# Performance work log

Hardware: AMD Instinct MI355X
Metric: run time of the kernel (lower is better)

Reference implementation:

```python
import jax, jax.numpy as jnp
import numpy as np

H = 1024        # hidden_units
NH = 16         # num_heads
HD = H // NH    # head_dim = 64
B = 32
S = 500
MAX_SEQ = 500
ROPE_BASE = 10000.0


def setup_inputs() -> dict:
    key = jax.random.key(0)
    ks = jax.random.split(key, 16)
    s = 1.0 / np.sqrt(H)
    inp = {
        "query": jax.random.normal(ks[0], (B, S, H), jnp.float32),
        "key":   jax.random.normal(ks[1], (B, S, H), jnp.float32),
        "value": jax.random.normal(ks[2], (B, S, H), jnp.float32),
        "attn_mask": jax.random.randint(ks[3], (B, S), 0, 2).astype(bool),
        "Wq": jax.random.uniform(ks[4], (H, H), jnp.float32, -s, s),
        "bq": jax.random.uniform(ks[5], (H,), jnp.float32, -s, s),
        "Wk": jax.random.uniform(ks[6], (H, H), jnp.float32, -s, s),
        "bk": jax.random.uniform(ks[7], (H,), jnp.float32, -s, s),
        "Wv": jax.random.uniform(ks[8], (H, H), jnp.float32, -s, s),
        "bv": jax.random.uniform(ks[9], (H,), jnp.float32, -s, s),
        "Wo": jax.random.uniform(ks[10], (H, H), jnp.float32, -s, s),
        "bo": jax.random.uniform(ks[11], (H,), jnp.float32, -s, s),
        # rel_pos_bias embedding table: [2*max_seq_len-1, num_heads]
        "rel_emb": jax.random.normal(ks[12], (2 * MAX_SEQ - 1, NH), jnp.float32),
    }
    return inp


def _rope_tables(seq_len, head_dim, dtype):
    inv_freq = 1.0 / (ROPE_BASE ** (jnp.arange(0, head_dim, 2, dtype=jnp.float32) / head_dim))
    t = jnp.arange(seq_len, dtype=jnp.float32)
    freqs = t[:, None] * inv_freq[None, :]           # [S, HD/2]
    emb = jnp.concatenate([freqs, freqs], axis=-1)   # [S, HD]
    return jnp.cos(emb).astype(dtype), jnp.sin(emb).astype(dtype)


def _apply_rope(x, cos, sin):
    # x: [B, NH, S, HD]; even/odd slicing variant from source
    x_rot = jnp.concatenate([-x[..., 1::2], x[..., 0::2]], axis=-1)
    return x * cos + x_rot * sin


def reference(query, key, value, attn_mask, Wq, bq, Wk, bk, Wv, bv, Wo, bo, rel_emb):
    b, s, _ = query.shape
    Q = (query @ Wq.T + bq).reshape(b, s, NH, HD).transpose(0, 2, 1, 3)  # [B,NH,S,HD]
    K = (key   @ Wk.T + bk).reshape(b, s, NH, HD).transpose(0, 2, 1, 3)
    V = (value @ Wv.T + bv).reshape(b, s, NH, HD).transpose(0, 2, 1, 3)

    cos, sin = _rope_tables(s, HD, Q.dtype)  # [S,HD]
    Q = _apply_rope(Q, cos, sin)
    K = _apply_rope(K, cos, sin)

    # relative-position bias: [1, NH, S, S]
    pos = jnp.arange(s)[:, None] - jnp.arange(s)[None, :]
    rel_idx = jnp.clip(pos + MAX_SEQ - 1, 0, 2 * MAX_SEQ - 2)
    rel_bias = rel_emb[rel_idx].transpose(2, 0, 1)[None]  # [1,NH,S,S]

    # key-padding mask -> additive float mask [B,1,1,S]
    mask_bias = jnp.where(attn_mask[:, None, None, :], 0.0, -jnp.inf).astype(Q.dtype)

    scale = 1.0 / np.sqrt(HD)
    scores = jnp.einsum('bhqd,bhkd->bhqk', Q, K) * scale + mask_bias + rel_bias
    attn = jax.nn.softmax(scores, axis=-1)
    out = jnp.einsum('bhqk,bhkd->bhqd', attn, V)
    out = out.transpose(0, 2, 1, 3).reshape(b, s, H)
    out = jnp.clip(out, -30.0, 30.0)
    return out @ Wo.T + bo
```

## Files before the change

### kernel.cpp

```cpp
#include <hip/hip_runtime.h>
#include <math.h>


typedef unsigned short u16;
typedef unsigned int   u32;
typedef unsigned char  u8;
using bf16x8 = __attribute__((ext_vector_type(8))) short;
using f32x4  = __attribute__((ext_vector_type(4))) float;
using f32x2  = __attribute__((ext_vector_type(2))) float;
using u16x4  = __attribute__((ext_vector_type(4))) unsigned short;

#define DEV __device__ __forceinline__

#if __has_builtin(__builtin_amdgcn_exp2f)
#define EXP2(x) __builtin_amdgcn_exp2f(x)
#else
#define EXP2(x) exp2f(x)
#endif

DEV u16 f2bf(float f) {
  union { float f; u32 u; } c; c.f = f;
  u32 u = c.u;
  return (u16)((u + 0x7FFFu + ((u >> 16) & 1u)) >> 16);
}
DEV float bf2f(u16 h) {
  union { u32 u; float f; } c; c.u = ((u32)h) << 16;
  return c.f;
}
DEV u32 cvtpk(float a, float b) {
  u32 r;
  asm("v_cvt_pk_bf16_f32 %0, %1, %2" : "=v"(r) : "v"(a), "v"(b));
  return r;
}

DEV void async16(void* l, const void* g) {
  __builtin_amdgcn_global_load_lds(
      (__attribute__((address_space(1))) unsigned int*)g,
      (__attribute__((address_space(3))) unsigned int*)l, 16, 0, 0);
}

__global__ __launch_bounds__(512) void build_gather(const void* __restrict__ mraw,
                                                    u16* __restrict__ karr,
                                                    int* __restrict__ kept) {
  const int b = blockIdx.x;
  const int t = threadIdx.x;
  const int lane = t & 63, wave = t >> 6;
  __shared__ int s_li, s_lf;
  __shared__ int wbase[8];
  __shared__ int wpop[8];
  if (t == 0) { s_li = 0; s_lf = 0; }
  __syncthreads();
  const u32* w = (const u32*)mraw;
  int li = 0, lf = 0;
  for (int g = t; g < 4000; g += 512) {
    u32 v = w[g];
    li |= !(v == 0u || v == 1u);
    lf |= !(v == 0u || v == 0x3F800000u);
  }
  if (li) atomicOr(&s_li, 1);
  if (lf) atomicOr(&s_lf, 1);
  __syncthreads();
  const int mode = (!s_li) ? 0 : ((!s_lf) ? 1 : 2);
  int v = 0;
  if (t < 500) {
    if (mode == 0)      v = ((const int*)mraw)[b * 500 + t] != 0;
    else if (mode == 1) v = (((const float*)mraw)[b * 500 + t] != 0.0f);
    else                v = ((const u8*)mraw)[b * 500 + t] != 0;
  }
  unsigned long long bal = __ballot(v != 0);
  karr[b * 512 + t] = 0xFFFF;
  if (lane == 0) wpop[wave] = __popcll(bal);
  __syncthreads();
  if (t == 0) {
    int s = 0;
    for (int ww = 0; ww < 8; ++ww) { wbase[ww] = s; s += wpop[ww]; }
    kept[b] = s;
  }
  __syncthreads();
  if (v) {
    int rank = wbase[wave] + __popcll(bal & ((1ull << lane) - 1ull));
    karr[b * 512 + rank] = (u16)t;
  }
}

__global__ __launch_bounds__(256) void rope_table(float* __restrict__ tab) {
  int idx = blockIdx.x * 256 + threadIdx.x;
  if (idx >= 16000) return;
  int s = idx >> 5, j = idx & 31;
  float ang = (float)s * exp2f(-(float)j * 0.41524100f);
  float sn, cs;
  sincosf(ang, &sn, &cs);
  tab[idx * 2] = cs;
  tab[idx * 2 + 1] = sn;
}

__global__ __launch_bounds__(256) void cvt_w4(const float* __restrict__ w0,
                                              const float* __restrict__ w1,
                                              const float* __restrict__ w2,
                                              const float* __restrict__ w3,
                                              u16* __restrict__ dst) {
  const float* src = (blockIdx.y == 0) ? w0 : (blockIdx.y == 1) ? w1
                    : (blockIdx.y == 2) ? w2 : w3;
  int i = blockIdx.x * 256 + threadIdx.x;
  f32x4 f = *(const f32x4*)(src + (size_t)i * 4);
  u16x4 o;
  o[0] = f2bf(f[0]); o[1] = f2bf(f[1]); o[2] = f2bf(f[2]); o[3] = f2bf(f[3]);
  *(u16x4*)(dst + (size_t)blockIdx.y * 1048576 + (size_t)i * 4) = o;
}

__global__ __launch_bounds__(256) void cvt_f32_bf16(const float* __restrict__ src,
                                                    u16* __restrict__ dst, int n4) {
  int i = blockIdx.x * 256 + threadIdx.x;
  int stride = gridDim.x * 256;
  for (; i < n4; i += stride) {
    f32x4 f = *(const f32x4*)(src + (size_t)i * 4);
    u16x4 o;
    o[0] = f2bf(f[0]); o[1] = f2bf(f[1]); o[2] = f2bf(f[2]); o[3] = f2bf(f[3]);
    *(u16x4*)(dst + (size_t)i * 4) = o;
  }
}

__global__ __launch_bounds__(256) void gathercvt2(const float* __restrict__ srcK,
                                                  const float* __restrict__ srcV,
                                                  const u16* __restrict__ karr,
                                                  const int* __restrict__ kept,
                                                  u16* __restrict__ dstK,
                                                  u16* __restrict__ dstV) {
  const int b = blockIdx.y;
  const int r = blockIdx.x * 2 + (threadIdx.x >> 7);
  if (r >= kept[b]) return;
  const float* src = blockIdx.z ? srcV : srcK;
  u16* dst = blockIdx.z ? dstV : dstK;
  const int c = (threadIdx.x & 127) * 8;
  const int tok = karr[b * 512 + r];
  const float* s = src + ((size_t)b * 500 + tok) * 1024 + c;
  f32x4 f0 = *(const f32x4*)s;
  f32x4 f1 = *(const f32x4*)(s + 4);
  u16 o[8];
  o[0] = f2bf(f0[0]); o[1] = f2bf(f0[1]); o[2] = f2bf(f0[2]); o[3] = f2bf(f0[3]);
  o[4] = f2bf(f1[0]); o[5] = f2bf(f1[1]); o[6] = f2bf(f1[2]); o[7] = f2bf(f1[3]);
  *(bf16x8*)(dst + ((size_t)b * 512 + r) * 1024 + c) = *(bf16x8*)o;
}

template <int MODE>
__global__ __launch_bounds__(512, 2) void gemm_bt(const u16* __restrict__ A,
                                                  const u16* __restrict__ Bw,
                                                  const float* __restrict__ bias,
                                                  void* __restrict__ Cout, int M,
                                                  const float* __restrict__ tabg,
                                                  const int* __restrict__ keptp) {
  const int bid = blockIdx.x;
  int m0, n0, Mloc;
  size_t abase, crowbase;
  if (MODE == 3) {
    const int swz = (bid & 7) * 32 + (bid >> 3);
    const int mb = swz >> 2;
    n0 = (swz & 3) * 256;
    const int b = mb >> 1, rb = mb & 1;
    const int kb = keptp[b];
    if (rb * 256 >= kb) return;
    m0 = rb * 256;
    Mloc = kb;
    abase = (size_t)b * 512 * 1024;
    crowbase = (size_t)b * 512;
  } else {
    const int xcd = bid & 7, idx = bid >> 3;
    const int swz = (xcd < 4 ? xcd * 32 : 128 + (xcd - 4) * 31) + idx;
    m0 = (swz >> 2) * 256;
    n0 = (swz & 3) * 256;
    Mloc = M;
    abase = 0;
    crowbase = 0;
  }
  const int tid = threadIdx.x;
  const int wave = tid >> 6;
  const int wr = wave >> 2, wc = wave & 3;
  const int fr = tid & 15, fo = (tid >> 4) & 3;
  const int sl0 = (fo ^ (fr & 7)) * 8;
  const int sl1 = ((4 + fo) ^ (fr & 7)) * 8;

  __shared__ __attribute__((aligned(16))) u16 AS[2 * 16384];
  __shared__ __attribute__((aligned(16))) u16 BS[2 * 16384];

  f32x4 acc[8][4];
#pragma unroll
  for (int mi = 0; mi < 8; ++mi)
#pragma unroll
    for (int ni = 0; ni < 4; ++ni)
#pragma unroll
      for (int j = 0; j < 4; ++j) acc[mi][ni][j] = 0.f;

  auto STG = [&](int t, int buf) {
    u16* sA = &AS[buf * 16384];
    u16* sB = &BS[buf * 16384];
#pragma unroll
    for (int i = 0; i < 4; ++i) {
      int c = i * 512 + tid;
      int r = c >> 3, v = (c & 7) ^ (r & 7);
      int ar = min(m0 + r, Mloc - 1);
      async16(&sA[c * 8], A + abase + (size_t)ar * 1024 + t * 64 + v * 8);
    }
#pragma unroll
    for (int i = 0; i < 4; ++i) {
      int c = i * 512 + tid;
      int r = c >> 3, v = (c & 7) ^ (r & 7);
      async16(&sB[c * 8], Bw + (size_t)(n0 + r) * 1024 + t * 64 + v * 8);
    }
  };

  STG(0, 0);
  asm volatile("s_waitcnt vmcnt(0)" ::: "memory");
  __builtin_amdgcn_sched_barrier(0);
  __builtin_amdgcn_s_barrier();

  int cur = 0;
  for (int t = 0; t < 16; ++t) {
    if (t + 1 < 16) STG(t + 1, cur ^ 1);
    const u16* a0 = &AS[cur * 16384];
    const u16* b0 = &BS[cur * 16384];
    bf16x8 a[8], b[4];
#pragma unroll
    for (int mi = 0; mi < 8; ++mi)
      a[mi] = *(const bf16x8*)&a0[(wr * 128 + mi * 16 + fr) * 64 + sl0];
#pragma unroll
    for (int ni = 0; ni < 4; ++ni)
      b[ni] = *(const bf16x8*)&b0[(wc * 64 + ni * 16 + fr) * 64 + sl0];
    asm volatile("s_waitcnt lgkmcnt(0)" ::: "memory");
    __builtin_amdgcn_sched_barrier(0);
    __builtin_amdgcn_s_setprio(1);
#pragma unroll
    for (int mi = 0; mi < 8; ++mi)
#pragma unroll
      for (int ni = 0; ni < 4; ++ni)
        acc[mi][ni] = __builtin_amdgcn_mfma_f32_16x16x32_bf16(a[mi], b[ni], acc[mi][ni], 0, 0, 0);
    __builtin_amdgcn_s_setprio(0);
#pragma unroll
    for (int mi = 0; mi < 8; ++mi)
      a[mi] = *(const bf16x8*)&a0[(wr * 128 + mi * 16 + fr) * 64 + sl1];
#pragma unroll
    for (int ni = 0; ni < 4; ++ni)
      b[ni] = *(const bf16x8*)&b0[(wc * 64 + ni * 16 + fr) * 64 + sl1];
    asm volatile("s_waitcnt lgkmcnt(0)" ::: "memory");
    __builtin_amdgcn_sched_barrier(0);
    __builtin_amdgcn_s_setprio(1);
#pragma unroll
    for (int mi = 0; mi < 8; ++mi)
#pragma unroll
      for (int ni = 0; ni < 4; ++ni)
        acc[mi][ni] = __builtin_amdgcn_mfma_f32_16x16x32_bf16(a[mi], b[ni], acc[mi][ni], 0, 0, 0);
    __builtin_amdgcn_s_setprio(0);
    asm volatile("s_waitcnt vmcnt(0)" ::: "memory");
    __builtin_amdgcn_sched_barrier(0);
    __builtin_amdgcn_s_barrier();
    cur ^= 1;
  }

  __syncthreads();
  if (MODE == 2) {
    float* fw = (float*)&AS[0] + wave * 1024;
    const int hh = (n0 >> 6) + wc;
    const int lane = tid & 63;
    const int row = lane >> 2;
    const int jb = (lane & 3) * 8;
    float bvv[4];
#pragma unroll
    for (int ni = 0; ni < 4; ++ni) bvv[ni] = bias[n0 + wc * 64 + ni * 16 + fr];
#pragma unroll
    for (int mi = 0; mi < 8; ++mi) {
#pragma unroll
      for (int ni = 0; ni < 4; ++ni)
#pragma unroll
        for (int r = 0; r < 4; ++r)
          fw[(fo * 4 + r) * 64 + ni * 16 + fr] = acc[mi][ni][r] + bvv[ni];
      int m = m0 + wr * 128 + mi * 16 + row;
      if (m < Mloc) {
        int bb = (u32)m / 500u;
        int ss = m - bb * 500;
        u16* dst = (u16*)Cout + (((size_t)(bb * 16 + hh)) * 500 + ss) * 64;
        bf16x8 va, vb;
#pragma unroll
        for (int p = 0; p < 8; ++p) {
          int j = jb + p;
          float x0 = fw[row * 64 + j];
          float x1 = fw[row * 64 + 32 + j];
          float xe = fw[row * 64 + 2 * j];
          float xo = fw[row * 64 + 2 * j + 1];
          f32x2 cn = *(const f32x2*)(tabg + (ss * 32 + j) * 2);
          va[p] = (short)f2bf(x0 * cn[0] - xo * cn[1]);
          vb[p] = (short)f2bf(x1 * cn[0] + xe * cn[1]);
        }
        *(bf16x8*)(dst + jb) = va;
        *(bf16x8*)(dst + 32 + jb) = vb;
      }
      __builtin_amdgcn_s_barrier();
    }
  } else if (MODE == 1 || MODE == 3) {
    u16* bw = (u16*)&AS[0] + wave * 2048;
#pragma unroll
    for (int mi = 0; mi < 8; ++mi) {
#pragma unroll
      for (int ni = 0; ni < 4; ++ni) {
        float bv = bias[n0 + wc * 64 + ni * 16 + fr];
#pragma unroll
        for (int r = 0; r < 4; ++r)
          bw[(fo * 4 + r) * 64 + ni * 16 + fr] = f2bf(acc[mi][ni][r] + bv);
      }
      int lane = tid & 63;
      int ro = lane >> 2, ch = lane & 3;
      int m = m0 + wr * 128 + mi * 16 + ro;
      bf16x8 v0 = *(const bf16x8*)&bw[ro * 64 + ch * 16];
      bf16x8 v1 = *(const bf16x8*)&bw[ro * 64 + ch * 16 + 8];
      if (m < Mloc) {
        u16* dst = (u16*)Cout + (crowbase + m) * 1024 + n0 + wc * 64 + ch * 16;
        *(bf16x8*)dst = v0;
        *(bf16x8*)(dst + 8) = v1;
      }
    }
  } else {
    float* fw = (float*)&AS[0] + wave * 1024;
#pragma unroll
    for (int mi = 0; mi < 8; ++mi) {
#pragma unroll
      for (int ni = 0; ni < 4; ++ni) {
        float bv = bias[n0 + wc * 64 + ni * 16 + fr];
#pragma unroll
        for (int r = 0; r < 4; ++r)
          fw[(fo * 4 + r) * 64 + ni * 16 + fr] = acc[mi][ni][r] + bv;
      }
      int lane = tid & 63;
      int ro = lane >> 2, ch = lane & 3;
      int m = m0 + wr * 128 + mi * 16 + ro;
      f32x4 v0 = *(const f32x4*)&fw[ro * 64 + ch * 16];
      f32x4 v1 = *(const f32x4*)&fw[ro * 64 + ch * 16 + 4];
      f32x4 v2 = *(const f32x4*)&fw[ro * 64 + ch * 16 + 8];
      f32x4 v3 = *(const f32x4*)&fw[ro * 64 + ch * 16 + 12];
      if (m < Mloc) {
        float* dst = (float*)Cout + (size_t)m * 1024 + n0 + wc * 64 + ch * 16;
        *(f32x4*)dst = v0;
        *(f32x4*)(dst + 4) = v1;
        *(f32x4*)(dst + 8) = v2;
        *(f32x4*)(dst + 12) = v3;
      }
    }
  }
}

__global__ __launch_bounds__(256) void gather_k(const u16* __restrict__ PkC,
                                                const float* __restrict__ tab,
                                                const u16* __restrict__ karr,
                                                const int* __restrict__ kept,
                                                u16* __restrict__ Ktg) {
  const int tile = blockIdx.x;
  const int bh = blockIdx.y;
  const int h = bh & 15, b = bh >> 4;
  if (tile * 64 >= kept[b]) return;
  char* out = (char*)(Ktg + ((size_t)bh * 8 + tile) * 4096);
  const int tid = threadIdx.x;
#pragma unroll
  for (int i = 0; i < 8; ++i) {
    int item = i * 256 + tid;
    int row = item >> 5, j = item & 31;
    int rk = tile * 64 + row;
    int tok = karr[b * 512 + rk];
    int sw = (row & 7) << 4;
    u16 o0 = 0, o1 = 0;
    if (tok != 0xFFFF) {
      const u16* src = PkC + ((size_t)b * 512 + rk) * 1024 + h * 64;
      float x0 = bf2f(src[j]);
      float x1 = bf2f(src[32 + j]);
      float xe = bf2f(src[2 * j]);
      float xo = bf2f(src[2 * j + 1]);
      f32x2 cn = *(const f32x2*)(tab + (tok * 32 + j) * 2);
      o0 = f2bf(x0 * cn[0] - xo * cn[1]);
      o1 = f2bf(x1 * cn[0] + xe * cn[1]);
    }
    *(u16*)(out + row * 128 + ((2 * j) ^ sw)) = o0;
    *(u16*)(out + row * 128 + ((64 + 2 * j) ^ sw)) = o1;
  }
}

__global__ __launch_bounds__(256) void gather_v(const u16* __restrict__ PvC,
                                                const u16* __restrict__ karr,
                                                const int* __restrict__ kept,
                                                u16* __restrict__ Vtg) {
  const int tile = blockIdx.x;
  const int bh = blockIdx.y;
  const int h = bh & 15, b = bh >> 4;
  if (tile * 64 >= kept[b]) return;
  const int tid = threadIdx.x;
  __shared__ __attribute__((aligned(16))) u16 Vl[64 * 64];
#pragma unroll
  for (int i = 0; i < 2; ++i) {
    int chunk = i * 256 + tid;
    int slot = chunk >> 3, seg = chunk & 7;
    int rk = tile * 64 + slot;
    int tok = karr[b * 512 + rk];
    bf16x8 v;
#pragma unroll
    for (int p = 0; p < 8; ++p) v[p] = 0;
    if (tok != 0xFFFF)
      v = *(const bf16x8*)(PvC + ((size_t)b * 512 + rk) * 1024 + h * 64 + seg * 8);
    *(bf16x8*)&Vl[slot * 64 + seg * 8] = v;
  }
  __syncthreads();
  u16* out = Vtg + ((size_t)bh * 8 + tile) * 4096;
#pragma unroll
  for (int i = 0; i < 2; ++i) {
    int chunk = i * 256 + tid;
    int d = chunk >> 3, c16 = chunk & 7;
    int k0 = ((c16 * 16) ^ ((d & 7) << 4)) >> 1;
    bf16x8 v;
#pragma unroll
    for (int p = 0; p < 8; ++p) v[p] = (short)Vl[(k0 + p) * 64 + d];
    *(bf16x8*)(out + chunk * 8) = v;
  }
}

__global__ __launch_bounds__(512) void attn_kernel(const u16* __restrict__ Qr,
                                                   const u16* __restrict__ Ktg,
                                                   const u16* __restrict__ Vtg,
                                                   const float* __restrict__ rel_emb,
                                                   const u16* __restrict__ karr,
                                                   const int* __restrict__ kept,
                                                   u16* __restrict__ AO) {
  const int bid = blockIdx.x;
  const int bh = ((bid >> 5) << 3) | (bid & 7);
  const int qb = (bid >> 3) & 3;
  const int h = bh & 15, b = bh >> 4;
  const int q0 = qb * 128;
  const int tid = threadIdx.x;
  const int wave = tid >> 6;
  const int fr = tid & 15, fo = (tid >> 4) & 3;

  __shared__ __attribute__((aligned(16))) u16 Ks[2][4096];
  __shared__ __attribute__((aligned(16))) u16 Vs[2][4096];
  __shared__ __attribute__((aligned(16))) u16 Pl[8][1024];
  __shared__ float rel2[640];
  __shared__ u16 okk[512];

  const int nt = (kept[b] + 63) >> 6;
  const float LOG2E = 1.44269504f;
  for (int i = tid; i < 640; i += 512) {
    int g = min(max(q0 - 12 + i, 0), 998);
    rel2[i] = (i == 0) ? -1e30f : rel_emb[g * 16 + h] * LOG2E;
  }
  okk[tid] = karr[b * 512 + tid];

  const int qloc = wave * 16 + fr;
  const int qc = qloc + 511;
  const u16* Qb = Qr + ((size_t)bh * 500 + min(q0 + qloc, 499)) * 64;
  bf16x8 qf0 = *(const bf16x8*)(Qb + fo * 8);
  bf16x8 qf1 = *(const bf16x8*)(Qb + 32 + fo * 8);

  f32x4 o[4];
#pragma unroll
  for (int nf = 0; nf < 4; ++nf)
#pragma unroll
    for (int j = 0; j < 4; ++j) o[nf][j] = 0.f;
  float mrun = -1e30f, lrun = 0.f;

  const u16* Kb = Ktg + (size_t)bh * 32768;
  const u16* Vb = Vtg + (size_t)bh * 32768;
  const int sw = (fr & 7) << 4;
  const float SC = 0.18033688f;

  if (nt > 0) {
    async16(&Ks[0][tid * 8], Kb + tid * 8);
    async16(&Vs[0][tid * 8], Vb + tid * 8);
  }
  __syncthreads();

  for (int t = 0; t < nt; ++t) {
    const int cur = t & 1;
    if (t + 1 < nt) {
      async16(&Ks[cur ^ 1][tid * 8], Kb + (t + 1) * 4096 + tid * 8);
      async16(&Vs[cur ^ 1][tid * 8], Vb + (t + 1) * 4096 + tid * 8);
    }
    const char* Kt = (const char*)(cur ? &Ks[1][0] : &Ks[0][0]);
    const char* Vt = (const char*)(cur ? &Vs[1][0] : &Vs[0][0]);

    f32x4 sacc[4];
    __builtin_amdgcn_s_setprio(1);
#pragma unroll
    for (int nf = 0; nf < 4; ++nf) {
#pragma unroll
      for (int jj = 0; jj < 4; ++jj) sacc[nf][jj] = 0.f;
      int rb = (nf * 16 + fr) * 128;
      bf16x8 kb0 = *(const bf16x8*)(Kt + rb + ((fo * 16) ^ sw));
      bf16x8 kb1 = *(const bf16x8*)(Kt + rb + ((64 + fo * 16) ^ sw));
      sacc[nf] = __builtin_amdgcn_mfma_f32_16x16x32_bf16(kb0, qf0, sacc[nf], 0, 0, 0);
      sacc[nf] = __builtin_amdgcn_mfma_f32_16x16x32_bf16(kb1, qf1, sacc[nf], 0, 0, 0);
    }
    __builtin_amdgcn_s_setprio(0);

    float p2[4][4];
    float pmax = -3e30f;
#pragma unroll
    for (int nf = 0; nf < 4; ++nf) {
      u16x4 ok4 = *(const u16x4*)&okk[t * 64 + nf * 16 + fo * 4];
#pragma unroll
      for (int r = 0; r < 4; ++r) {
        int idx2 = max(qc - (int)ok4[r], 0);
        float s2 = fmaf(sacc[nf][r], SC, rel2[idx2]);
        p2[nf][r] = s2;
        pmax = fmaxf(pmax, s2);
      }
    }
    pmax = fmaxf(pmax, __shfl_xor(pmax, 16, 64));
    pmax = fmaxf(pmax, __shfl_xor(pmax, 32, 64));

    if (!__all(pmax <= mrun + 8.0f)) {
      float mnew = fmaxf(mrun, pmax);
      float scl = EXP2(mrun - mnew);
      lrun *= scl;
#pragma unroll
      for (int nf = 0; nf < 4; ++nf)
#pragma unroll
        for (int r = 0; r < 4; ++r) o[nf][r] *= scl;
      mrun = mnew;
    }

    float lsum = 0.f;
#pragma unroll
    for (int nf = 0; nf < 4; ++nf) {
      float e0 = EXP2(p2[nf][0] - mrun);
      float e1 = EXP2(p2[nf][1] - mrun);
      float e2 = EXP2(p2[nf][2] - mrun);
      float e3 = EXP2(p2[nf][3] - mrun);
      lsum += (e0 + e1) + (e2 + e3);
      uint2 w; w.x = cvtpk(e0, e1); w.y = cvtpk(e2, e3);
      *(uint2*)((char*)&Pl[wave][0] + fr * 128 + ((nf * 32 + fo * 8) ^ sw)) = w;
    }
    lsum += __shfl_xor(lsum, 16, 64);
    lsum += __shfl_xor(lsum, 32, 64);
    lrun += lsum;

    bf16x8 pa0 = *(const bf16x8*)((char*)&Pl[wave][0] + fr * 128 + ((fo * 16) ^ sw));
    bf16x8 pa1 = *(const bf16x8*)((char*)&Pl[wave][0] + fr * 128 + ((64 + fo * 16) ^ sw));
    __builtin_amdgcn_s_setprio(1);
#pragma unroll
    for (int nf = 0; nf < 4; ++nf) {
      int rb = (nf * 16 + fr) * 128;
      bf16x8 vb0 = *(const bf16x8*)(Vt + rb + ((fo * 16) ^ sw));
      bf16x8 vb1 = *(const bf16x8*)(Vt + rb + ((64 + fo * 16) ^ sw));
      o[nf] = __builtin_amdgcn_mfma_f32_16x16x32_bf16(vb0, pa0, o[nf], 0, 0, 0);
      o[nf] = __builtin_amdgcn_mfma_f32_16x16x32_bf16(vb1, pa1, o[nf], 0, 0, 0);
    }
    __builtin_amdgcn_s_setprio(0);
    __syncthreads();
  }

  float inv = (lrun > 0.f) ? 1.f / lrun : 0.f;
#pragma unroll
  for (int nf = 0; nf < 4; ++nf) {
    float v0 = fminf(fmaxf(o[nf][0] * inv, -30.f), 30.f);
    float v1 = fminf(fmaxf(o[nf][1] * inv, -30.f), 30.f);
    float v2 = fminf(fmaxf(o[nf][2] * inv, -30.f), 30.f);
    float v3 = fminf(fmaxf(o[nf][3] * inv, -30.f), 30.f);
    uint2 w; w.x = cvtpk(v0, v1); w.y = cvtpk(v2, v3);
    *(uint2*)((char*)&Pl[wave][0] + fr * 128 + ((nf * 32 + fo * 8) ^ sw)) = w;
  }
  {
    int lane = tid & 63;
    int ro = lane >> 2, c = lane & 3;
    int swr = (ro & 7) << 4;
    const char* Pw = (const char*)&Pl[wave][0];
    bf16x8 v0 = *(const bf16x8*)(Pw + ro * 128 + ((c * 32) ^ swr));
    bf16x8 v1 = *(const bf16x8*)(Pw + ro * 128 + ((c * 32 + 16) ^ swr));
    int token = q0 + wave * 16 + ro;
    if (token < 500) {
      u16* dst = AO + (size_t)(b * 500 + token) * 1024 + h * 64 + c * 16;
      *(bf16x8*)dst = v0;
      *(bf16x8*)(dst + 8) = v1;
    }
  }
}

extern "C" void kernel_launch(void* const* d_in, const int* in_sizes, int n_in,
                              void* d_out, int out_size, void* d_ws, size_t ws_size,
                              hipStream_t stream) {
  const float* query = (const float*)d_in[0];
  const float* key_  = (const float*)d_in[1];
  const float* value = (const float*)d_in[2];
  const void*  mask  = d_in[3];
  const float* Wq = (const float*)d_in[4];
  const float* bq = (const float*)d_in[5];
  const float* Wk = (const float*)d_in[6];
  const float* bk = (const float*)d_in[7];
  const float* Wv = (const float*)d_in[8];
  const float* bv = (const float*)d_in[9];
  const float* Wo = (const float*)d_in[10];
  const float* bo = (const float*)d_in[11];
  const float* rel = (const float*)d_in[12];

  char* ws = (char*)d_ws;
  const size_t SLOT = 33554432;
  u16* Wb = (u16*)ws;
  char* Aq = ws + 8388608;
  char* Bq = Aq + SLOT;
  char* Cq = Bq + SLOT;
  char* Dq = Cq + SLOT;
  char* MISC = Dq + SLOT;
  u16* karr  = (u16*)(MISC + 65536);
  int* kept  = (int*)(MISC + 131072);
  float* tab = (float*)(MISC + 131584);

  build_gather<<<32, 512, 0, stream>>>(mask, karr, kept);
  rope_table<<<63, 256, 0, stream>>>(tab);
  cvt_w4<<<dim3(1024, 4), 256, 0, stream>>>(Wq, Wk, Wv, Wo, Wb);
  cvt_f32_bf16<<<2048, 256, 0, stream>>>(query, (u16*)Aq, 4096000);
  gathercvt2<<<dim3(256, 32, 2), 256, 0, stream>>>(key_, value, karr, kept,
                                                   (u16*)Bq, (u16*)Cq);

  gemm_bt<3><<<256, 512, 0, stream>>>((u16*)Cq, Wb + 2 * 1048576, bv, Dq, 0, tab, kept);
  gemm_bt<2><<<252, 512, 0, stream>>>((u16*)Aq, Wb + 0 * 1048576, bq, Cq, 16000, tab, nullptr);
  gemm_bt<3><<<256, 512, 0, stream>>>((u16*)Bq, Wb + 1 * 1048576, bk, Aq, 0, tab, kept);

  gather_k<<<dim3(8, 512), 256, 0, stream>>>((u16*)Aq, tab, karr, kept, (u16*)Bq);
  gather_v<<<dim3(8, 512), 256, 0, stream>>>((u16*)Dq, karr, kept, (u16*)Aq);

  attn_kernel<<<2048, 512, 0, stream>>>((u16*)Cq, (u16*)Bq, (u16*)Aq, rel,
                                        karr, kept, (u16*)Dq);

  gemm_bt<0><<<252, 512, 0, stream>>>((u16*)Dq, Wb + 3 * 1048576, bo, (float*)d_out, 16000, tab, nullptr);
}
```

Before: 297.3 us.

## Shrink GEMM tiles to 256x128 with K32 stages for higher occupancy

The bf16 projection GEMMs change from 256x256 output tiles with 64-wide K stages to 256x128 tiles with 32-wide K stages. Pairs of rows are packed into each 64-element LDS row, with a new swizzle. Per-wave accumulators halve, and the launch bound rises to 4 blocks per CU, so the grids double and the XCD swizzle is recomputed. The aim is more resident waves to hide latency and better CU load balance. In exchange there is less operand reuse per tile and twice as many barrier-separated K iterations.

```diff
diff --git a/kernel.cpp b/kernel.cpp
--- a/kernel.cpp
+++ b/kernel.cpp
@@ -143,7 +143,7 @@
 }
 
 template <int MODE>
-__global__ __launch_bounds__(512, 2) void gemm_bt(const u16* __restrict__ A,
+__global__ __launch_bounds__(512, 4) void gemm_bt(const u16* __restrict__ A,
                                                   const u16* __restrict__ Bw,
                                                   const float* __restrict__ bias,
                                                   void* __restrict__ Cout, int M,
@@ -153,9 +153,9 @@
   int m0, n0, Mloc;
   size_t abase, crowbase;
   if (MODE == 3) {
-    const int swz = (bid & 7) * 32 + (bid >> 3);
-    const int mb = swz >> 2;
-    n0 = (swz & 3) * 256;
+    const int swz = (bid & 7) * 64 + (bid >> 3);
+    const int mb = swz >> 3;
+    n0 = (swz & 7) * 128;
     const int b = mb >> 1, rb = mb & 1;
     const int kb = keptp[b];
     if (rb * 256 >= kb) return;
@@ -164,47 +164,48 @@
     abase = (size_t)b * 512 * 1024;
     crowbase = (size_t)b * 512;
   } else {
-    const int xcd = bid & 7, idx = bid >> 3;
-    const int swz = (xcd < 4 ? xcd * 32 : 128 + (xcd - 4) * 31) + idx;
-    m0 = (swz >> 2) * 256;
-    n0 = (swz & 3) * 256;
+    const int swz = (bid & 7) * 63 + (bid >> 3);
+    m0 = (swz >> 3) * 256;
+    n0 = (swz & 7) * 128;
     Mloc = M;
     abase = 0;
     crowbase = 0;
   }
   const int tid = threadIdx.x;
   const int wave = tid >> 6;
-  const int wr = wave >> 2, wc = wave & 3;
+  const int wr = wave >> 1, wc = wave & 1;
   const int fr = tid & 15, fo = (tid >> 4) & 3;
-  const int sl0 = (fo ^ (fr & 7)) * 8;
-  const int sl1 = ((4 + fo) ^ (fr & 7)) * 8;
-
-  __shared__ __attribute__((aligned(16))) u16 AS[2 * 16384];
-  __shared__ __attribute__((aligned(16))) u16 BS[2 * 16384];
-
-  f32x4 acc[8][4];
-#pragma unroll
-  for (int mi = 0; mi < 8; ++mi)
+  const int fr2 = fr >> 1;
+  const int aslot = ((4 * (fr & 1) + fo) ^ fr2) * 8;
+
+  const int ATILE = 128 * 64;
+  const int BTILE = 64 * 64;
+  __shared__ __attribute__((aligned(16))) u16 AS[2 * 128 * 64];
+  __shared__ __attribute__((aligned(16))) u16 BS[2 * 64 * 64];
+
+  f32x4 acc[4][4];
+#pragma unroll
+  for (int mi = 0; mi < 4; ++mi)
 #pragma unroll
     for (int ni = 0; ni < 4; ++ni)
 #pragma unroll
       for (int j = 0; j < 4; ++j) acc[mi][ni][j] = 0.f;
 
   auto STG = [&](int t, int buf) {
-    u16* sA = &AS[buf * 16384];
-    u16* sB = &BS[buf * 16384];
-#pragma unroll
-    for (int i = 0; i < 4; ++i) {
+    u16* sA = &AS[buf * ATILE];
+    u16* sB = &BS[buf * BTILE];
+#pragma unroll
+    for (int i = 0; i < 2; ++i) {
       int c = i * 512 + tid;
       int r = c >> 3, v = (c & 7) ^ (r & 7);
-      int ar = min(m0 + r, Mloc - 1);
-      async16(&sA[c * 8], A + abase + (size_t)ar * 1024 + t * 64 + v * 8);
-    }
-#pragma unroll
-    for (int i = 0; i < 4; ++i) {
-      int c = i * 512 + tid;
+      int ar = min(m0 + 2 * r + (v >> 2), Mloc - 1);
+      async16(&sA[c * 8], A + abase + (size_t)ar * 1024 + t * 32 + (v & 3) * 8);
+    }
+    {
+      int c = tid;
       int r = c >> 3, v = (c & 7) ^ (r & 7);
-      async16(&sB[c * 8], Bw + (size_t)(n0 + r) * 1024 + t * 64 + v * 8);
+      int nr = n0 + 2 * r + (v >> 2);
+      async16(&sB[c * 8], Bw + (size_t)nr * 1024 + t * 32 + (v & 3) * 8);
     }
   };
 
@@ -214,37 +215,22 @@
   __builtin_amdgcn_s_barrier();
 
   int cur = 0;
-  for (int t = 0; t < 16; ++t) {
-    if (t + 1 < 16) STG(t + 1, cur ^ 1);
-    const u16* a0 = &AS[cur * 16384];
-    const u16* b0 = &BS[cur * 16384];
-    bf16x8 a[8], b[4];
-#pragma unroll
-    for (int mi = 0; mi < 8; ++mi)
-      a[mi] = *(const bf16x8*)&a0[(wr * 128 + mi * 16 + fr) * 64 + sl0];
+  for (int t = 0; t < 32; ++t) {
+    if (t + 1 < 32) STG(t + 1, cur ^ 1);
+    const u16* a0 = &AS[cur * ATILE];
+    const u16* b0 = &BS[cur * BTILE];
+    bf16x8 a[4], b[4];
+#pragma unroll
+    for (int mi = 0; mi < 4; ++mi)
+      a[mi] = *(const bf16x8*)&a0[(wr * 32 + mi * 8 + fr2) * 64 + aslot];
 #pragma unroll
     for (int ni = 0; ni < 4; ++ni)
-      b[ni] = *(const bf16x8*)&b0[(wc * 64 + ni * 16 + fr) * 64 + sl0];
+      b[ni] = *(const bf16x8*)&b0[(wc * 32 + ni * 8 + fr2) * 64 + aslot];
     asm volatile("s_waitcnt lgkmcnt(0)" ::: "memory");
     __builtin_amdgcn_sched_barrier(0);
     __builtin_amdgcn_s_setprio(1);
 #pragma unroll
-    for (int mi = 0; mi < 8; ++mi)
-#pragma unroll
-      for (int ni = 0; ni < 4; ++ni)
-        acc[mi][ni] = __builtin_amdgcn_mfma_f32_16x16x32_bf16(a[mi], b[ni], acc[mi][ni], 0, 0, 0);
-    __builtin_amdgcn_s_setprio(0);
-#pragma unroll
-    for (int mi = 0; mi < 8; ++mi)
-      a[mi] = *(const bf16x8*)&a0[(wr * 128 + mi * 16 + fr) * 64 + sl1];
-#pragma unroll
-    for (int ni = 0; ni < 4; ++ni)
-      b[ni] = *(const bf16x8*)&b0[(wc * 64 + ni * 16 + fr) * 64 + sl1];
-    asm volatile("s_waitcnt lgkmcnt(0)" ::: "memory");
-    __builtin_amdgcn_sched_barrier(0);
-    __builtin_amdgcn_s_setprio(1);
-#pragma unroll
-    for (int mi = 0; mi < 8; ++mi)
+    for (int mi = 0; mi < 4; ++mi)
 #pragma unroll
       for (int ni = 0; ni < 4; ++ni)
         acc[mi][ni] = __builtin_amdgcn_mfma_f32_16x16x32_bf16(a[mi], b[ni], acc[mi][ni], 0, 0, 0);
@@ -266,13 +252,13 @@
 #pragma unroll
     for (int ni = 0; ni < 4; ++ni) bvv[ni] = bias[n0 + wc * 64 + ni * 16 + fr];
 #pragma unroll
-    for (int mi = 0; mi < 8; ++mi) {
+    for (int mi = 0; mi < 4; ++mi) {
 #pragma unroll
       for (int ni = 0; ni < 4; ++ni)
 #pragma unroll
         for (int r = 0; r < 4; ++r)
           fw[(fo * 4 + r) * 64 + ni * 16 + fr] = acc[mi][ni][r] + bvv[ni];
-      int m = m0 + wr * 128 + mi * 16 + row;
+      int m = m0 + wr * 64 + mi * 16 + row;
       if (m < Mloc) {
         int bb = (u32)m / 500u;
         int ss = m - bb * 500;
@@ -297,7 +283,7 @@
   } else if (MODE == 1 || MODE == 3) {
     u16* bw = (u16*)&AS[0] + wave * 2048;
 #pragma unroll
-    for (int mi = 0; mi < 8; ++mi) {
+    for (int mi = 0; mi < 4; ++mi) {
 #pragma unroll
       for (int ni = 0; ni < 4; ++ni) {
         float bv = bias[n0 + wc * 64 + ni * 16 + fr];
@@ -307,7 +293,7 @@
       }
       int lane = tid & 63;
       int ro = lane >> 2, ch = lane & 3;
-      int m = m0 + wr * 128 + mi * 16 + ro;
+      int m = m0 + wr * 64 + mi * 16 + ro;
       bf16x8 v0 = *(const bf16x8*)&bw[ro * 64 + ch * 16];
       bf16x8 v1 = *(const bf16x8*)&bw[ro * 64 + ch * 16 + 8];
       if (m < Mloc) {
@@ -319,7 +305,7 @@
   } else {
     float* fw = (float*)&AS[0] + wave * 1024;
 #pragma unroll
-    for (int mi = 0; mi < 8; ++mi) {
+    for (int mi = 0; mi < 4; ++mi) {
 #pragma unroll
       for (int ni = 0; ni < 4; ++ni) {
         float bv = bias[n0 + wc * 64 + ni * 16 + fr];
@@ -329,7 +315,7 @@
       }
       int lane = tid & 63;
       int ro = lane >> 2, ch = lane & 3;
-      int m = m0 + wr * 128 + mi * 16 + ro;
+      int m = m0 + wr * 64 + mi * 16 + ro;
       f32x4 v0 = *(const f32x4*)&fw[ro * 64 + ch * 16];
       f32x4 v1 = *(const f32x4*)&fw[ro * 64 + ch * 16 + 4];
       f32x4 v2 = *(const f32x4*)&fw[ro * 64 + ch * 16 + 8];
@@ -612,9 +598,9 @@
   gathercvt2<<<dim3(256, 32, 2), 256, 0, stream>>>(key_, value, karr, kept,
                                                    (u16*)Bq, (u16*)Cq);
 
-  gemm_bt<3><<<256, 512, 0, stream>>>((u16*)Cq, Wb + 2 * 1048576, bv, Dq, 0, tab, kept);
-  gemm_bt<2><<<252, 512, 0, stream>>>((u16*)Aq, Wb + 0 * 1048576, bq, Cq, 16000, tab, nullptr);
-  gemm_bt<3><<<256, 512, 0, stream>>>((u16*)Bq, Wb + 1 * 1048576, bk, Aq, 0, tab, kept);
+  gemm_bt<3><<<512, 512, 0, stream>>>((u16*)Cq, Wb + 2 * 1048576, bv, Dq, 0, tab, kept);
+  gemm_bt<2><<<504, 512, 0, stream>>>((u16*)Aq, Wb + 0 * 1048576, bq, Cq, 16000, tab, nullptr);
+  gemm_bt<3><<<512, 512, 0, stream>>>((u16*)Bq, Wb + 1 * 1048576, bk, Aq, 0, tab, kept);
 
   gather_k<<<dim3(8, 512), 256, 0, stream>>>((u16*)Aq, tab, karr, kept, (u16*)Bq);
   gather_v<<<dim3(8, 512), 256, 0, stream>>>((u16*)Dq, karr, kept, (u16*)Aq);
@@ -622,5 +608,5 @@
   attn_kernel<<<2048, 512, 0, stream>>>((u16*)Cq, (u16*)Bq, (u16*)Aq, rel,
                                         karr, kept, (u16*)Dq);
 
-  gemm_bt<0><<<252, 512, 0, stream>>>((u16*)Dq, Wb + 3 * 1048576, bo, (float*)d_out, 16000, tab, nullptr);
-}
+  gemm_bt<0><<<504, 512, 0, stream>>>((u16*)Dq, Wb + 3 * 1048576, bo, (float*)d_out, 16000, tab, nullptr);
+}
```

Measured after the change: 292.0 us. About the same (-1.8%).
